# Performance work log

Hardware: AMD Instinct MI355X
Metric: run time of the kernel (lower is better)

The kernel has to match this reference:

```python
import jax, jax.numpy as jnp
import numpy as np


def setup_inputs() -> dict:
    key = jax.random.key(0)
    k1, k2 = jax.random.split(key)
    B, S, D = 16, 2048, 128
    x1 = jax.random.normal(k1, (B, S, D), dtype=jnp.float32)
    x2 = jax.random.normal(k2, (B, S, D), dtype=jnp.float32)
    return {"x1": x1, "x2": x2}


def reference(x1, x2):
    # Mutual cross attention (eval mode, dropout is identity).
    d = x1.shape[-1]
    scale = 1.0 / jnp.sqrt(jnp.asarray(d, dtype=x1.dtype))
    # scores[b,i,j] = <x1[b,i], x2[b,j]> / sqrt(d). The second score matrix in the
    # original (key @ query^T) is exactly the transpose, so compute once.
    scores = jnp.einsum("bid,bjd->bij", x1, x2) * scale  # [B,S,S]
    out_A = jnp.einsum("bij,bjd->bid", jax.nn.softmax(scores, axis=-1), x2)
    # softmax over rows of scores^T == softmax over axis -2 of scores, then transpose
    out_B = jnp.einsum("bij,bid->bjd", jax.nn.softmax(scores, axis=-2), x1)
    return out_A + out_B
```

## Files before the change

kernel.cpp:

```cpp
#include <hip/hip_runtime.h>

typedef _Float16 f16;
typedef f16 f16x2 __attribute__((ext_vector_type(2)));
typedef f16 f16x4 __attribute__((ext_vector_type(4)));
typedef f16 f16x8 __attribute__((ext_vector_type(8)));
typedef float f32x16 __attribute__((ext_vector_type(16)));
typedef unsigned int u32;

#define MFMA32(a, b, c) __builtin_amdgcn_mfma_f32_32x32x16_f16((a), (b), (c), 0, 0, 0)

namespace {
constexpr int SN = 2048;
constexpr int DN = 128;
constexpr int KVB = 64;
constexpr int NT = SN / KVB;
constexpr int QB = 128;
constexpr int TILE_E = KVB * DN;
constexpr float SCALE_L2E = 0.1275213897f;
constexpr float CLAMP = 14.0f;
}

__device__ __forceinline__ int kidx(int kv, int d) { return kv * DN + (d ^ ((kv & 7) << 3)); }
__device__ __forceinline__ int vidx(int d, int kv) { return d * KVB + (kv ^ (((d ^ (d >> 3)) & 7) << 3)); }

__device__ __forceinline__ void gl_lds16(const f16* g, f16* l) {
    __builtin_amdgcn_global_load_lds(
        (const __attribute__((address_space(1))) void*)g,
        (__attribute__((address_space(3))) void*)l, 16, 0, 0);
}

__global__ __launch_bounds__(256)
void prep_kernel(const float* __restrict__ x1, const float* __restrict__ x2,
                 f16* __restrict__ prepK, f16* __restrict__ prepV)
{
    const int gid  = blockIdx.x;
    const int pass = gid >> 9;
    const int b    = (gid >> 5) & 15;
    const int tile = gid & 31;
    const float* src = (pass ? x1 : x2) + ((size_t)b * SN + (size_t)tile * KVB) * DN;
    f16* outK = prepK + (size_t)gid * TILE_E;
    f16* outV = prepV + (size_t)gid * TILE_E;

    const int t   = threadIdx.x;
    const int kvg = t >> 5;
    const int dg  = t & 31;

    float hv[8][4];
    #pragma unroll
    for (int rr = 0; rr < 8; ++rr) {
        float4 a = *(const float4*)(src + (8 * kvg + rr) * DN + 4 * dg);
        hv[rr][0] = a.x; hv[rr][1] = a.y; hv[rr][2] = a.z; hv[rr][3] = a.w;
    }
    #pragma unroll
    for (int rr = 0; rr < 8; ++rr) {
        f16x4 kp;
        #pragma unroll
        for (int j = 0; j < 4; ++j) kp[j] = (f16)hv[rr][j];
        *(f16x4*)&outK[kidx(8 * kvg + rr, 4 * dg)] = kp;
    }
    #pragma unroll
    for (int i = 0; i < 4; ++i) {
        f16x8 vp;
        #pragma unroll
        for (int rr = 0; rr < 8; ++rr) vp[rr] = (f16)hv[rr][i];
        *(f16x8*)&outV[vidx(4 * dg + i, 8 * kvg)] = vp;
    }
}

__global__ __launch_bounds__(256, 2)
void mca_fast(const float* __restrict__ x1, const float* __restrict__ x2,
              const f16* __restrict__ prepK, const f16* __restrict__ prepV,
              float* __restrict__ out)
{
    __shared__ __align__(16) f16 sK[2][TILE_E];
    __shared__ __align__(16) f16 sV[3][TILE_E];

    const int gid  = blockIdx.x;
    const int work = (gid & 7) * 64 + (gid >> 3);
    const int pass = work >> 8;
    const int b    = (work >> 4) & 15;
    const int q0   = (work & 15) * QB;

    const int t  = threadIdx.x;
    const int w  = t >> 6;
    const int l  = t & 63;
    const int lq = l & 31;
    const int hi = l >> 5;

    const float* xq = pass ? x2 : x1;
    const float* qp = xq + ((size_t)b * SN + q0 + w * 32 + lq) * DN;
    const f16* gK = prepK + ((size_t)((pass * 16 + b) * 32)) * TILE_E;
    const f16* gV = prepV + ((size_t)((pass * 16 + b) * 32)) * TILE_E;

    f16x8 qf[8];
    #pragma unroll
    for (int c = 0; c < 8; ++c) {
        const float* p = qp + 16 * c + 8 * hi;
        float4 a0 = *(const float4*)p;
        float4 a1 = *(const float4*)(p + 4);
        f16x8 q;
        q[0] = (f16)(a0.x * SCALE_L2E); q[1] = (f16)(a0.y * SCALE_L2E);
        q[2] = (f16)(a0.z * SCALE_L2E); q[3] = (f16)(a0.w * SCALE_L2E);
        q[4] = (f16)(a1.x * SCALE_L2E); q[5] = (f16)(a1.y * SCALE_L2E);
        q[6] = (f16)(a1.z * SCALE_L2E); q[7] = (f16)(a1.w * SCALE_L2E);
        qf[c] = q;
    }

    auto STAGE = [&](int kb, int vb, int tile) {
        const f16* srcK = gK + (size_t)tile * TILE_E + t * 8;
        const f16* srcV = gV + (size_t)tile * TILE_E + t * 8;
        #pragma unroll
        for (int i = 0; i < 4; ++i) {
            gl_lds16(srcK + i * 2048, &sK[kb][i * 2048 + t * 8]);
            gl_lds16(srcV + i * 2048, &sV[vb][i * 2048 + t * 8]);
        }
    };

    f32x16 oAcc[4] = {{}, {}, {}, {}};
    float lsum[16];
    #pragma unroll
    for (int r = 0; r < 16; ++r) lsum[r] = 0.f;
    f16x8 pf[4] = {{}, {}, {}, {}};

    auto PVH = [&](const f16* Vb, int db0, int db1) {
        __builtin_amdgcn_s_setprio(1);
        #pragma unroll
        for (int db = 0; db < 4; ++db) {
            if (db < db0 || db >= db1) continue;
            #pragma unroll
            for (int f = 0; f < 4; ++f) {
                f16x8 va = *(const f16x8*)&Vb[vidx(db * 32 + lq, f * 16 + 8 * hi)];
                oAcc[db] = MFMA32(va, pf[f], oAcc[db]);
            }
        }
        __builtin_amdgcn_s_setprio(0);
    };

    STAGE(0, 0, 0);
    STAGE(1, 1, 1);

    int vprev = 2, vcur = 0, vst = 2;

    for (int tile = 0; tile < NT; ++tile) {
        const int kcur = tile & 1;

        if (tile > 0) PVH(sV[vprev], 0, 2);

        if (tile < NT - 1) asm volatile("s_waitcnt vmcnt(8)" ::: "memory");
        else               asm volatile("s_waitcnt vmcnt(0)" ::: "memory");
        asm volatile("s_barrier" ::: "memory");

        f32x16 sacc[2] = {{}, {}};
        __builtin_amdgcn_s_setprio(1);
        #pragma unroll
        for (int c = 0; c < 8; ++c) {
            f16x8 ka0 = *(const f16x8*)&sK[kcur][kidx(lq,      16 * c + 8 * hi)];
            f16x8 ka1 = *(const f16x8*)&sK[kcur][kidx(32 + lq, 16 * c + 8 * hi)];
            sacc[0] = MFMA32(ka0, qf[c], sacc[0]);
            sacc[1] = MFMA32(ka1, qf[c], sacc[1]);
        }
        __builtin_amdgcn_s_setprio(0);

        if (tile > 0) PVH(sV[vprev], 2, 4);

        {
            float p[32];
            #pragma unroll
            for (int kvb = 0; kvb < 2; ++kvb)
                #pragma unroll
                for (int r = 0; r < 16; ++r) {
                    float pv = exp2f(fminf(sacc[kvb][r], CLAMP));
                    p[kvb * 16 + r] = pv;
                    lsum[r] += pv;
                }
            #pragma unroll
            for (int f = 0; f < 4; ++f) {
                const int base = (f >> 1) * 16 + (f & 1) * 8;
                u32 wd[4];
                #pragma unroll
                for (int W = 0; W < 2; ++W) {
                    union { f16x2 h; u32 u; } A, B;
                    A.h[0] = (f16)p[base + 2 * W];     A.h[1] = (f16)p[base + 2 * W + 1];
                    B.h[0] = (f16)p[base + 2 * W + 4]; B.h[1] = (f16)p[base + 2 * W + 5];
                    u32 xA = (u32)__shfl_xor((int)A.u, 32);
                    u32 xB = (u32)__shfl_xor((int)B.u, 32);
                    wd[W]     = hi ? xB : A.u;
                    wd[W + 2] = hi ? B.u : xA;
                }
                union { u32 u[4]; f16x8 v; } cvt;
                cvt.u[0] = wd[0]; cvt.u[1] = wd[1]; cvt.u[2] = wd[2]; cvt.u[3] = wd[3];
                pf[f] = cvt.v;
            }
        }

        asm volatile("s_barrier" ::: "memory");
        if (tile + 2 < NT) STAGE(kcur, vst, tile + 2);

        vprev = vcur;
        vcur  = (vcur == 2) ? 0 : vcur + 1;
        vst   = (vst  == 2) ? 0 : vst  + 1;
    }

    PVH(sV[vprev], 0, 4);

    #pragma unroll
    for (int s = 8; s >= 1; s >>= 1)
        #pragma unroll
        for (int r = 0; r < s; ++r) lsum[r] += lsum[r + s];
    const float L = lsum[0] + __shfl_xor(lsum[0], 32);
    const float inv = 1.0f / L;

    __syncthreads();

    float* sO = (w < 2) ? ((float*)sK) + w * (32 * 128)
                        : ((float*)sV) + (w - 2) * (32 * 128);
    #pragma unroll
    for (int db = 0; db < 4; ++db)
        #pragma unroll
        for (int rr = 0; rr < 4; ++rr) {
            const int d0 = db * 32 + rr * 8 + hi * 4;
            float4 st;
            st.x = oAcc[db][rr * 4 + 0] * inv;
            st.y = oAcc[db][rr * 4 + 1] * inv;
            st.z = oAcc[db][rr * 4 + 2] * inv;
            st.w = oAcc[db][rr * 4 + 3] * inv;
            *(float4*)&sO[lq * 128 + (d0 ^ ((lq & 7) << 2))] = st;
        }
    float* ob = out + ((size_t)b * SN + q0 + w * 32) * DN;
    #pragma unroll 4
    for (int q = 0; q < 32; ++q) {
        const int sw = (q & 7) << 2;
        float v0 = sO[q * 128 + (l ^ sw)];
        float v1 = sO[q * 128 + ((l + 64) ^ sw)];
        atomicAdd(&ob[q * DN + l], v0);
        atomicAdd(&ob[q * DN + 64 + l], v1);
    }
}

__global__ __launch_bounds__(256, 2)
void mca_fallback(const float* __restrict__ x1, const float* __restrict__ x2,
                  float* __restrict__ out)
{
    __shared__ __align__(16) f16 sK[2][KVB * DN];
    __shared__ __align__(16) f16 sV[2][DN * KVB];

    const int gid  = blockIdx.x;
    const int work = (gid & 7) * 64 + (gid >> 3);
    const int pass = work >> 8;
    const int b    = (work >> 4) & 15;
    const int q0   = (work & 15) * QB;

    const int t  = threadIdx.x;
    const int w  = t >> 6;
    const int l  = t & 63;
    const int lq = l & 31;
    const int hi = l >> 5;
    const int kvg = t >> 5;
    const int dg  = t & 31;

    const float* xq  = pass ? x2 : x1;
    const float* xkv = pass ? x1 : x2;
    const float* qp  = xq + ((size_t)b * SN + q0 + w * 32 + lq) * DN;
    const float* kb  = xkv + (size_t)b * SN * DN;

    f16x8 qf[8];
    #pragma unroll
    for (int c = 0; c < 8; ++c) {
        const float* p = qp + 16 * c + 8 * hi;
        float4 a0 = *(const float4*)p;
        float4 a1 = *(const float4*)(p + 4);
        f16x8 q;
        q[0] = (f16)(a0.x * SCALE_L2E); q[1] = (f16)(a0.y * SCALE_L2E);
        q[2] = (f16)(a0.z * SCALE_L2E); q[3] = (f16)(a0.w * SCALE_L2E);
        q[4] = (f16)(a1.x * SCALE_L2E); q[5] = (f16)(a1.y * SCALE_L2E);
        q[6] = (f16)(a1.z * SCALE_L2E); q[7] = (f16)(a1.w * SCALE_L2E);
        qf[c] = q;
    }

    float hv[8][4];
    auto LOAD = [&](int tile) {
        const float* src = kb + ((size_t)tile * KVB + 8 * kvg) * DN + 4 * dg;
        #pragma unroll
        for (int rr = 0; rr < 8; ++rr) {
            float4 a = *(const float4*)(src + rr * DN);
            hv[rr][0] = a.x; hv[rr][1] = a.y; hv[rr][2] = a.z; hv[rr][3] = a.w;
        }
    };
    auto WRITE = [&](int buf) {
        #pragma unroll
        for (int rr = 0; rr < 8; ++rr) {
            f16x4 kp;
            #pragma unroll
            for (int j = 0; j < 4; ++j) kp[j] = (f16)hv[rr][j];
            *(f16x4*)&sK[buf][kidx(8 * kvg + rr, 4 * dg)] = kp;
        }
        #pragma unroll
        for (int i = 0; i < 4; ++i) {
            f16x8 vp;
            #pragma unroll
            for (int rr = 0; rr < 8; ++rr) vp[rr] = (f16)hv[rr][i];
            *(f16x8*)&sV[buf][vidx(4 * dg + i, 8 * kvg)] = vp;
        }
    };

    f32x16 oAcc[4] = {{}, {}, {}, {}};
    float lsum[16];
    #pragma unroll
    for (int r = 0; r < 16; ++r) lsum[r] = 0.f;

    LOAD(0); WRITE(0);
    __syncthreads();

    for (int tile = 0; tile < NT; ++tile) {
        const int cur = tile & 1;
        if (tile + 1 < NT) LOAD(tile + 1);

        f32x16 sacc[2] = {{}, {}};
        __builtin_amdgcn_s_setprio(1);
        #pragma unroll
        for (int c = 0; c < 8; ++c) {
            f16x8 ka0 = *(const f16x8*)&sK[cur][kidx(lq,      16 * c + 8 * hi)];
            f16x8 ka1 = *(const f16x8*)&sK[cur][kidx(32 + lq, 16 * c + 8 * hi)];
            sacc[0] = MFMA32(ka0, qf[c], sacc[0]);
            sacc[1] = MFMA32(ka1, qf[c], sacc[1]);
        }
        __builtin_amdgcn_s_setprio(0);

        float p[32];
        #pragma unroll
        for (int kvb = 0; kvb < 2; ++kvb)
            #pragma unroll
            for (int r = 0; r < 16; ++r) {
                float pv = exp2f(fminf(sacc[kvb][r], CLAMP));
                p[kvb * 16 + r] = pv;
                lsum[r] += pv;
            }

        f16x8 pf[4];
        #pragma unroll
        for (int f = 0; f < 4; ++f) {
            const int base = (f >> 1) * 16 + (f & 1) * 8;
            u32 wd[4];
            #pragma unroll
            for (int W = 0; W < 2; ++W) {
                union { f16x2 h; u32 u; } A, B;
                A.h[0] = (f16)p[base + 2 * W];     A.h[1] = (f16)p[base + 2 * W + 1];
                B.h[0] = (f16)p[base + 2 * W + 4]; B.h[1] = (f16)p[base + 2 * W + 5];
                u32 xA = (u32)__shfl_xor((int)A.u, 32);
                u32 xB = (u32)__shfl_xor((int)B.u, 32);
                wd[W]     = hi ? xB : A.u;
                wd[W + 2] = hi ? B.u : xA;
            }
            union { u32 u[4]; f16x8 v; } cvt;
            cvt.u[0] = wd[0]; cvt.u[1] = wd[1]; cvt.u[2] = wd[2]; cvt.u[3] = wd[3];
            pf[f] = cvt.v;
        }

        if (tile + 1 < NT) WRITE(cur ^ 1);

        __builtin_amdgcn_s_setprio(1);
        #pragma unroll
        for (int db = 0; db < 4; ++db) {
            #pragma unroll
            for (int f = 0; f < 4; ++f) {
                f16x8 va = *(const f16x8*)&sV[cur][vidx(db * 32 + lq, f * 16 + 8 * hi)];
                oAcc[db] = MFMA32(va, pf[f], oAcc[db]);
            }
        }
        __builtin_amdgcn_s_setprio(0);

        __syncthreads();
    }

    #pragma unroll
    for (int s = 8; s >= 1; s >>= 1)
        #pragma unroll
        for (int r = 0; r < s; ++r) lsum[r] += lsum[r + s];
    const float L = lsum[0] + __shfl_xor(lsum[0], 32);
    const float inv = 1.0f / L;

    __syncthreads();

    float* sO = (w < 2) ? ((float*)sK) + w * (32 * 128)
                        : ((float*)sV) + (w - 2) * (32 * 128);
    #pragma unroll
    for (int db = 0; db < 4; ++db)
        #pragma unroll
        for (int rr = 0; rr < 4; ++rr) {
            const int d0 = db * 32 + rr * 8 + hi * 4;
            float4 st;
            st.x = oAcc[db][rr * 4 + 0] * inv;
            st.y = oAcc[db][rr * 4 + 1] * inv;
            st.z = oAcc[db][rr * 4 + 2] * inv;
            st.w = oAcc[db][rr * 4 + 3] * inv;
            *(float4*)&sO[lq * 128 + (d0 ^ ((lq & 7) << 2))] = st;
        }
    float* ob = out + ((size_t)b * SN + q0 + w * 32) * DN;
    #pragma unroll 4
    for (int q = 0; q < 32; ++q) {
        const int sw = (q & 7) << 2;
        float v0 = sO[q * 128 + (l ^ sw)];
        float v1 = sO[q * 128 + ((l + 64) ^ sw)];
        atomicAdd(&ob[q * DN + l], v0);
        atomicAdd(&ob[q * DN + 64 + l], v1);
    }
}

extern "C" void kernel_launch(void* const* d_in, const int* in_sizes, int n_in,
                              void* d_out, int out_size, void* d_ws, size_t ws_size,
                              hipStream_t stream) {
    const float* x1 = (const float*)d_in[0];
    const float* x2 = (const float*)d_in[1];
    float* out = (float*)d_out;
    const int B = in_sizes[0] / (SN * DN);
    const size_t out_bytes = (size_t)out_size * sizeof(float);

    hipMemsetAsync(d_out, 0, out_bytes, stream);

    const size_t prep_elems = 2ull * 16 * 32 * TILE_E;
    const size_t need = 2ull * prep_elems * sizeof(f16);
    if (ws_size >= need) {
        f16* prepK = (f16*)d_ws;
        f16* prepV = prepK + prep_elems;
        hipLaunchKernelGGL(prep_kernel, dim3(1024), dim3(256), 0, stream,
                           x1, x2, prepK, prepV);
        hipLaunchKernelGGL(mca_fast, dim3(2 * B * (SN / QB)), dim3(256), 0, stream,
                           x1, x2, prepK, prepV, out);
    } else {
        hipLaunchKernelGGL(mca_fallback, dim3(2 * B * (SN / QB)), dim3(256), 0, stream,
                           x1, x2, out);
    }
}
```

Baseline: 141.4 us.

## Load V fragments directly from global and compute row sums via MFMA

Stops staging V tiles through LDS. Each wave now reads its V fragments straight from global/L2 using a plain, unswizzled prep layout, and only K goes through the LDS double buffer. The softmax denominator is no longer kept as per-lane scalar sums with a final reduction; an extra MFMA against an all-ones operand accumulates it. This cuts LDS traffic and frees the third V buffer, but the P·V MFMAs now wait on global-load latency with no prefetch. The earlier PV/QK interleaving across tiles is also removed.

```diff
diff --git a/kernel.cpp b/kernel.cpp
--- a/kernel.cpp
+++ b/kernel.cpp
@@ -21,7 +21,6 @@
 }
 
 __device__ __forceinline__ int kidx(int kv, int d) { return kv * DN + (d ^ ((kv & 7) << 3)); }
-__device__ __forceinline__ int vidx(int d, int kv) { return d * KVB + (kv ^ (((d ^ (d >> 3)) & 7) << 3)); }
 
 __device__ __forceinline__ void gl_lds16(const f16* g, f16* l) {
     __builtin_amdgcn_global_load_lds(
@@ -63,7 +62,7 @@
         f16x8 vp;
         #pragma unroll
         for (int rr = 0; rr < 8; ++rr) vp[rr] = (f16)hv[rr][i];
-        *(f16x8*)&outV[vidx(4 * dg + i, 8 * kvg)] = vp;
+        *(f16x8*)&outV[(4 * dg + i) * KVB + 8 * kvg] = vp;
     }
 }
 
@@ -72,8 +71,8 @@
               const f16* __restrict__ prepK, const f16* __restrict__ prepV,
               float* __restrict__ out)
 {
-    __shared__ __align__(16) f16 sK[2][TILE_E];
-    __shared__ __align__(16) f16 sV[3][TILE_E];
+    __shared__ __align__(16) unsigned char smem[65536];
+    f16* sK = (f16*)smem;
 
     const int gid  = blockIdx.x;
     const int work = (gid & 7) * 64 + (gid >> 3);
@@ -106,73 +105,49 @@
         qf[c] = q;
     }
 
-    auto STAGE = [&](int kb, int vb, int tile) {
+    f16x8 ones;
+    #pragma unroll
+    for (int j = 0; j < 8; ++j) ones[j] = (f16)1.0f;
+
+    auto STAGE_K = [&](int buf, int tile) {
         const f16* srcK = gK + (size_t)tile * TILE_E + t * 8;
-        const f16* srcV = gV + (size_t)tile * TILE_E + t * 8;
-        #pragma unroll
-        for (int i = 0; i < 4; ++i) {
-            gl_lds16(srcK + i * 2048, &sK[kb][i * 2048 + t * 8]);
-            gl_lds16(srcV + i * 2048, &sV[vb][i * 2048 + t * 8]);
-        }
+        f16* dst = sK + buf * TILE_E + t * 8;
+        #pragma unroll
+        for (int i = 0; i < 4; ++i)
+            gl_lds16(srcK + i * 2048, dst + i * 2048);
     };
 
     f32x16 oAcc[4] = {{}, {}, {}, {}};
-    float lsum[16];
-    #pragma unroll
-    for (int r = 0; r < 16; ++r) lsum[r] = 0.f;
-    f16x8 pf[4] = {{}, {}, {}, {}};
-
-    auto PVH = [&](const f16* Vb, int db0, int db1) {
-        __builtin_amdgcn_s_setprio(1);
-        #pragma unroll
-        for (int db = 0; db < 4; ++db) {
-            if (db < db0 || db >= db1) continue;
-            #pragma unroll
-            for (int f = 0; f < 4; ++f) {
-                f16x8 va = *(const f16x8*)&Vb[vidx(db * 32 + lq, f * 16 + 8 * hi)];
-                oAcc[db] = MFMA32(va, pf[f], oAcc[db]);
-            }
-        }
-        __builtin_amdgcn_s_setprio(0);
-    };
-
-    STAGE(0, 0, 0);
-    STAGE(1, 1, 1);
-
-    int vprev = 2, vcur = 0, vst = 2;
+    f32x16 lacc = {};
+
+    STAGE_K(0, 0);
+    STAGE_K(1, 1);
 
     for (int tile = 0; tile < NT; ++tile) {
         const int kcur = tile & 1;
 
-        if (tile > 0) PVH(sV[vprev], 0, 2);
-
-        if (tile < NT - 1) asm volatile("s_waitcnt vmcnt(8)" ::: "memory");
-        else               asm volatile("s_waitcnt vmcnt(0)" ::: "memory");
+        asm volatile("s_waitcnt vmcnt(4)" ::: "memory");
         asm volatile("s_barrier" ::: "memory");
 
         f32x16 sacc[2] = {{}, {}};
         __builtin_amdgcn_s_setprio(1);
         #pragma unroll
         for (int c = 0; c < 8; ++c) {
-            f16x8 ka0 = *(const f16x8*)&sK[kcur][kidx(lq,      16 * c + 8 * hi)];
-            f16x8 ka1 = *(const f16x8*)&sK[kcur][kidx(32 + lq, 16 * c + 8 * hi)];
+            f16x8 ka0 = *(const f16x8*)&sK[kcur * TILE_E + kidx(lq,      16 * c + 8 * hi)];
+            f16x8 ka1 = *(const f16x8*)&sK[kcur * TILE_E + kidx(32 + lq, 16 * c + 8 * hi)];
             sacc[0] = MFMA32(ka0, qf[c], sacc[0]);
             sacc[1] = MFMA32(ka1, qf[c], sacc[1]);
         }
         __builtin_amdgcn_s_setprio(0);
 
-        if (tile > 0) PVH(sV[vprev], 2, 4);
-
+        f16x8 pf[4];
         {
             float p[32];
             #pragma unroll
             for (int kvb = 0; kvb < 2; ++kvb)
                 #pragma unroll
-                for (int r = 0; r < 16; ++r) {
-                    float pv = exp2f(fminf(sacc[kvb][r], CLAMP));
-                    p[kvb * 16 + r] = pv;
-                    lsum[r] += pv;
-                }
+                for (int r = 0; r < 16; ++r)
+                    p[kvb * 16 + r] = exp2f(fminf(sacc[kvb][r], CLAMP));
             #pragma unroll
             for (int f = 0; f < 4; ++f) {
                 const int base = (f >> 1) * 16 + (f & 1) * 8;
@@ -193,27 +168,34 @@
             }
         }
 
+        const f16* vt = gV + (size_t)tile * TILE_E;
+        f16x8 va[16];
+        #pragma unroll
+        for (int db = 0; db < 4; ++db)
+            #pragma unroll
+            for (int f = 0; f < 4; ++f)
+                va[db * 4 + f] = *(const f16x8*)&vt[(db * 32 + lq) * KVB + f * 16 + 8 * hi];
+
+        __builtin_amdgcn_s_setprio(1);
+        #pragma unroll
+        for (int f = 0; f < 4; ++f) lacc = MFMA32(ones, pf[f], lacc);
+        #pragma unroll
+        for (int db = 0; db < 4; ++db) {
+            #pragma unroll
+            for (int f = 0; f < 4; ++f)
+                oAcc[db] = MFMA32(va[db * 4 + f], pf[f], oAcc[db]);
+        }
+        __builtin_amdgcn_s_setprio(0);
+
         asm volatile("s_barrier" ::: "memory");
-        if (tile + 2 < NT) STAGE(kcur, vst, tile + 2);
-
-        vprev = vcur;
-        vcur  = (vcur == 2) ? 0 : vcur + 1;
-        vst   = (vst  == 2) ? 0 : vst  + 1;
-    }
-
-    PVH(sV[vprev], 0, 4);
-
-    #pragma unroll
-    for (int s = 8; s >= 1; s >>= 1)
-        #pragma unroll
-        for (int r = 0; r < s; ++r) lsum[r] += lsum[r + s];
-    const float L = lsum[0] + __shfl_xor(lsum[0], 32);
-    const float inv = 1.0f / L;
+        if (tile + 2 < NT) STAGE_K(kcur, tile + 2);
+    }
+
+    const float inv = 1.0f / lacc[0];
 
     __syncthreads();
 
-    float* sO = (w < 2) ? ((float*)sK) + w * (32 * 128)
-                        : ((float*)sV) + (w - 2) * (32 * 128);
+    float* sO = (float*)smem + w * (32 * 128);
     #pragma unroll
     for (int db = 0; db < 4; ++db)
         #pragma unroll
@@ -241,8 +223,8 @@
 void mca_fallback(const float* __restrict__ x1, const float* __restrict__ x2,
                   float* __restrict__ out)
 {
-    __shared__ __align__(16) f16 sK[2][KVB * DN];
-    __shared__ __align__(16) f16 sV[2][DN * KVB];
+    __shared__ __align__(16) f16 sKf[2][KVB * DN];
+    __shared__ __align__(16) f16 sVf[2][DN * KVB];
 
     const int gid  = blockIdx.x;
     const int work = (gid & 7) * 64 + (gid >> 3);
@@ -262,6 +244,8 @@
     const float* xkv = pass ? x1 : x2;
     const float* qp  = xq + ((size_t)b * SN + q0 + w * 32 + lq) * DN;
     const float* kb  = xkv + (size_t)b * SN * DN;
+
+    auto vidx = [](int d, int kv) { return d * KVB + (kv ^ (((d ^ (d >> 3)) & 7) << 3)); };
 
     f16x8 qf[8];
     #pragma unroll
@@ -292,14 +276,14 @@
             f16x4 kp;
             #pragma unroll
             for (int j = 0; j < 4; ++j) kp[j] = (f16)hv[rr][j];
-            *(f16x4*)&sK[buf][kidx(8 * kvg + rr, 4 * dg)] = kp;
+            *(f16x4*)&sKf[buf][kidx(8 * kvg + rr, 4 * dg)] = kp;
         }
         #pragma unroll
         for (int i = 0; i < 4; ++i) {
             f16x8 vp;
             #pragma unroll
             for (int rr = 0; rr < 8; ++rr) vp[rr] = (f16)hv[rr][i];
-            *(f16x8*)&sV[buf][vidx(4 * dg + i, 8 * kvg)] = vp;
+            *(f16x8*)&sVf[buf][vidx(4 * dg + i, 8 * kvg)] = vp;
         }
     };
 
@@ -319,8 +303,8 @@
         __builtin_amdgcn_s_setprio(1);
         #pragma unroll
         for (int c = 0; c < 8; ++c) {
-            f16x8 ka0 = *(const f16x8*)&sK[cur][kidx(lq,      16 * c + 8 * hi)];
-            f16x8 ka1 = *(const f16x8*)&sK[cur][kidx(32 + lq, 16 * c + 8 * hi)];
+            f16x8 ka0 = *(const f16x8*)&sKf[cur][kidx(lq,      16 * c + 8 * hi)];
+            f16x8 ka1 = *(const f16x8*)&sKf[cur][kidx(32 + lq, 16 * c + 8 * hi)];
             sacc[0] = MFMA32(ka0, qf[c], sacc[0]);
             sacc[1] = MFMA32(ka1, qf[c], sacc[1]);
         }
@@ -363,8 +347,8 @@
         for (int db = 0; db < 4; ++db) {
             #pragma unroll
             for (int f = 0; f < 4; ++f) {
-                f16x8 va = *(const f16x8*)&sV[cur][vidx(db * 32 + lq, f * 16 + 8 * hi)];
-                oAcc[db] = MFMA32(va, pf[f], oAcc[db]);
+                f16x8 vaf = *(const f16x8*)&sVf[cur][vidx(db * 32 + lq, f * 16 + 8 * hi)];
+                oAcc[db] = MFMA32(vaf, pf[f], oAcc[db]);
             }
         }
         __builtin_amdgcn_s_setprio(0);
@@ -381,8 +365,8 @@
 
     __syncthreads();
 
-    float* sO = (w < 2) ? ((float*)sK) + w * (32 * 128)
-                        : ((float*)sV) + (w - 2) * (32 * 128);
+    float* sO = (w < 2) ? ((float*)sKf) + w * (32 * 128)
+                        : ((float*)sVf) + (w - 2) * (32 * 128);
     #pragma unroll
     for (int db = 0; db < 4; ++db)
         #pragma unroll
```

Result: slower. 179.7 us (+27.1%).
